# Optimization experiments

Measured on AMD Instinct MI355X. Metric: run time of the kernel, lower is better.

The kernel has to match this reference:

```python
import jax, jax.numpy as jnp
import numpy as np

B, N, S, C, H = 8, 1024, 1024, 768, 12
D = C // H  # head dim 64
SCALE = D ** -0.5


def setup_inputs() -> dict:
    key = jax.random.key(0)
    ks = jax.random.split(key, 9)
    init = 0.02
    return {
        "query": jax.random.normal(ks[0], (B, N, C), jnp.float32),
        "key": jax.random.normal(ks[1], (B, S, C), jnp.float32),
        "value": jax.random.normal(ks[2], (B, S, C), jnp.float32),
        "attn_weight": jax.random.normal(ks[3], (B, H, N, S), jnp.float32),
        "Wq": jax.random.normal(ks[4], (C, C), jnp.float32) * init,
        "Wk": jax.random.normal(ks[5], (C, C), jnp.float32) * init,
        "Wv": jax.random.normal(ks[6], (C, C), jnp.float32) * init,
        "Wo": jax.random.normal(ks[7], (C, C), jnp.float32) * init,
        "bo": jnp.zeros((C,), jnp.float32),
    }


def reference(query, key, value, attn_weight, Wq, Wk, Wv, Wo, bo):
    # projections; torch Linear uses y = x @ W.T
    q = (query @ Wq.T).reshape(B, N, H, D).transpose(0, 2, 1, 3)  # b h n d
    k = (key @ Wk.T).reshape(B, S, H, D).transpose(0, 2, 1, 3)    # b h s d
    v = (value @ Wv.T).reshape(B, S, H, D).transpose(0, 2, 1, 3)  # b h s d

    scores = jnp.einsum("bhnd,bhsd->bhns", q, k) * SCALE          # [B,H,N,S]
    log_attn = jax.nn.log_softmax(scores, axis=-1)
    # bias-add then re-softmax (attn_weight path)
    logits = attn_weight + log_attn
    log_attn = logits
    attn = jax.nn.softmax(logits, axis=-1)

    out = jnp.einsum("bhns,bhsd->bhnd", attn, v)                   # [B,H,N,D]
    out = out.transpose(0, 2, 1, 3).reshape(B, N, C)               # b n (h d)
    out = out @ Wo.T + bo
    return out, log_attn
```

## Files before the change

### kernel.cpp

```cpp
#include <hip/hip_runtime.h>
#include <stdint.h>

#define DEV __device__ __forceinline__

typedef short bf16x8 __attribute__((ext_vector_type(8)));
typedef float f32x4 __attribute__((ext_vector_type(4)));

constexpr int CB = 8, CN = 1024, CS = 1024, CC = 768, CH = 12, CD = 64;

DEV unsigned short f32_to_bf16(float f) {
    unsigned int u = __builtin_bit_cast(unsigned int, f);
    u += 0x7fffu + ((u >> 16) & 1u);
    return (unsigned short)(u >> 16);
}
DEV float bf16_to_f32(unsigned short h) {
    return __builtin_bit_cast(float, (unsigned int)h << 16);
}

DEV uint4 load8_bf16(const float* __restrict__ src) {
    const float4 a = reinterpret_cast<const float4*>(src)[0];
    const float4 b = reinterpret_cast<const float4*>(src)[1];
    union { unsigned short s[8]; uint4 v; } u;
    u.s[0] = f32_to_bf16(a.x); u.s[1] = f32_to_bf16(a.y);
    u.s[2] = f32_to_bf16(a.z); u.s[3] = f32_to_bf16(a.w);
    u.s[4] = f32_to_bf16(b.x); u.s[5] = f32_to_bf16(b.y);
    u.s[6] = f32_to_bf16(b.z); u.s[7] = f32_to_bf16(b.w);
    return u.v;
}
DEV uint4 load8_bf16(const unsigned short* __restrict__ src) {
    return *reinterpret_cast<const uint4*>(src);
}

template<typename TA, typename TB, typename TC>
__global__ __launch_bounds__(256)
void gemm_nt(const TA* __restrict__ Ag, const TB* __restrict__ Bg, TC* __restrict__ Cg,
             int M, int Ndim, int K, int lda, int ldb, int Hb,
             long sAb, long sAh, long sBb, long sBh, long sCb, long sCh,
             long cSM, long cSN, float scale, const float* __restrict__ bias)
{
    const int bb = blockIdx.z / Hb;
    const int hh = blockIdx.z % Hb;
    const TA* __restrict__ A  = Ag + bb * sAb + hh * sAh;
    const TB* __restrict__ Bp = Bg + bb * sBb + hh * sBh;
    TC* __restrict__ C = Cg + bb * sCb + hh * sCh;

    const int tileM = blockIdx.x * 64;
    const int tileN = blockIdx.y * 64;
    const int tid  = threadIdx.x;
    const int lane = tid & 63;
    const int wv   = tid >> 6;
    const int wr   = (wv >> 1) * 32;
    const int wc   = (wv & 1) * 32;
    const int l15  = lane & 15;
    const int quad = lane >> 4;

    constexpr int LDP = 40;
    __shared__ unsigned short As[64 * LDP];
    __shared__ unsigned short Bs[64 * LDP];

    f32x4 acc[2][2] = {};

    const int ldRow = tid >> 2;
    const int ldCol = (tid & 3) * 8;

    const TA* aSrc = A  + (long)(tileM + ldRow) * lda + ldCol;
    const TB* bSrc = Bp + (long)(tileN + ldRow) * ldb + ldCol;
    uint4* aDst = reinterpret_cast<uint4*>(&As[ldRow * LDP + ldCol]);
    uint4* bDst = reinterpret_cast<uint4*>(&Bs[ldRow * LDP + ldCol]);

    for (int k0 = 0; k0 < K; k0 += 32) {
        *aDst = load8_bf16(aSrc + k0);
        *bDst = load8_bf16(bSrc + k0);
        __syncthreads();
        bf16x8 af[2], bfr[2];
        #pragma unroll
        for (int i = 0; i < 2; ++i)
            af[i] = *reinterpret_cast<const bf16x8*>(&As[(wr + i*16 + l15) * LDP + quad*8]);
        #pragma unroll
        for (int j = 0; j < 2; ++j)
            bfr[j] = *reinterpret_cast<const bf16x8*>(&Bs[(wc + j*16 + l15) * LDP + quad*8]);
        #pragma unroll
        for (int i = 0; i < 2; ++i)
            #pragma unroll
            for (int j = 0; j < 2; ++j)
                acc[i][j] = __builtin_amdgcn_mfma_f32_16x16x32_bf16(af[i], bfr[j], acc[i][j], 0, 0, 0);
        __syncthreads();
    }

    #pragma unroll
    for (int i = 0; i < 2; ++i) {
        #pragma unroll
        for (int j = 0; j < 2; ++j) {
            const int col = tileN + wc + j*16 + l15;
            const float bv = bias ? bias[col] : 0.0f;
            #pragma unroll
            for (int r = 0; r < 4; ++r) {
                const int row = tileM + wr + i*16 + quad*4 + r;
                const float v = acc[i][j][r] * scale + bv;
                const long idx = (long)row * cSM + (long)col * cSN;
                if constexpr (sizeof(TC) == 2) C[idx] = f32_to_bf16(v);
                else                           C[idx] = v;
            }
        }
    }
}

__global__ __launch_bounds__(256)
void softmax_k(const unsigned short* __restrict__ scores,
               const float* __restrict__ aw,
               float* __restrict__ log_attn,
               unsigned short* __restrict__ probs)
{
    const int lane = threadIdx.x & 63;
    const int wv   = threadIdx.x >> 6;
    const long row  = (long)blockIdx.x * 4 + wv;
    const long base = row * CS;

    float sc[16], t[16];
    #pragma unroll
    for (int j = 0; j < 16; ++j) {
        const int col = lane + j * 64;
        sc[j] = bf16_to_f32(scores[base + col]);
        t[j]  = aw[base + col] + sc[j];
    }
    float m1 = -3.4e38f, m2 = -3.4e38f;
    #pragma unroll
    for (int j = 0; j < 16; ++j) { m1 = fmaxf(m1, sc[j]); m2 = fmaxf(m2, t[j]); }
    #pragma unroll
    for (int off = 1; off < 64; off <<= 1) {
        m1 = fmaxf(m1, __shfl_xor(m1, off));
        m2 = fmaxf(m2, __shfl_xor(m2, off));
    }
    float l1 = 0.f, l2 = 0.f;
    #pragma unroll
    for (int j = 0; j < 16; ++j) { l1 += __expf(sc[j] - m1); l2 += __expf(t[j] - m2); }
    #pragma unroll
    for (int off = 1; off < 64; off <<= 1) {
        l1 += __shfl_xor(l1, off);
        l2 += __shfl_xor(l2, off);
    }
    const float lse1 = m1 + __logf(l1);
    const float inv2 = 1.0f / l2;
    #pragma unroll
    for (int j = 0; j < 16; ++j) {
        const int col = lane + j * 64;
        log_attn[base + col] = t[j] - lse1;
        probs[base + col]    = f32_to_bf16(__expf(t[j] - m2) * inv2);
    }
}

extern "C" void kernel_launch(void* const* d_in, const int* in_sizes, int n_in,
                              void* d_out, int out_size, void* d_ws, size_t ws_size,
                              hipStream_t stream)
{
    const float* query = (const float*)d_in[0];
    const float* key_  = (const float*)d_in[1];
    const float* value = (const float*)d_in[2];
    const float* aw    = (const float*)d_in[3];
    const float* Wq    = (const float*)d_in[4];
    const float* Wk    = (const float*)d_in[5];
    const float* Wv    = (const float*)d_in[6];
    const float* Wo    = (const float*)d_in[7];
    const float* bo    = (const float*)d_in[8];

    float* out      = (float*)d_out;
    float* log_attn = out + (long)CB * CN * CC;

    unsigned short* qproj = (unsigned short*)d_ws;
    unsigned short* kproj = qproj + (long)CB * CN * CC;
    unsigned short* vT    = kproj + (long)CB * CS * CC;
    unsigned short* sp    = vT    + (long)CB * CS * CC;
    unsigned short* aout  = sp    + (long)CB * CH * CN * CS;

    const dim3 blk(256);

    gemm_nt<float, float, unsigned short><<<dim3(128, 12, 1), blk, 0, stream>>>(
        query, Wq, qproj, CB*CN, CC, CC, CC, CC, 1,
        0, 0, 0, 0, 0, 0, (long)CC, 1, 1.0f, nullptr);
    gemm_nt<float, float, unsigned short><<<dim3(128, 12, 1), blk, 0, stream>>>(
        key_, Wk, kproj, CB*CS, CC, CC, CC, CC, 1,
        0, 0, 0, 0, 0, 0, (long)CC, 1, 1.0f, nullptr);
    gemm_nt<float, float, unsigned short><<<dim3(16, 12, 8), blk, 0, stream>>>(
        value, Wv, vT, CS, CC, CC, CC, CC, 1,
        (long)CS*CC, 0, 0, 0, (long)CH*CD*CS, 0, 1, (long)CS, 1.0f, nullptr);
    gemm_nt<unsigned short, unsigned short, unsigned short><<<dim3(16, 16, CB*CH), blk, 0, stream>>>(
        qproj, kproj, sp, CN, CS, CD, CC, CC, CH,
        (long)CN*CC, (long)CD, (long)CS*CC, (long)CD,
        (long)CH*CN*CS, (long)CN*CS, (long)CS, 1, 0.125f, nullptr);
    softmax_k<<<dim3(CB*CH*CN/4), blk, 0, stream>>>(sp, aw, log_attn, sp);
    gemm_nt<unsigned short, unsigned short, unsigned short><<<dim3(16, 1, CB*CH), blk, 0, stream>>>(
        sp, vT, aout, CN, CD, CS, CS, CS, CH,
        (long)CH*CN*CS, (long)CN*CS, (long)CH*CD*CS, (long)CD*CS,
        (long)CN*CC, (long)CD, (long)CC, 1, 1.0f, nullptr);
    gemm_nt<unsigned short, float, float><<<dim3(128, 12, 1), blk, 0, stream>>>(
        aout, Wo, out, CB*CN, CC, CC, CC, CC, 1,
        0, 0, 0, 0, 0, 0, (long)CC, 1, 1.0f, bo);
}
```

Baseline: 1.050 ms.

## Fuse QK^T, double softmax and PV into one LDS-resident attention kernel

Replaces the scores GEMM, the softmax kernel and the PV GEMM with one kernel per 32 query rows of a (batch, head). That kernel keeps the full 32x1024 bf16 score tile in swizzled shared memory. This removes the round trip of the B*H*N*S bf16 score and probability matrix through global memory. It also drops max subtraction in both softmaxes, relying on small score and bias magnitudes, which risks overflow for other inputs. The block uses 64KB of LDS, which limits occupancy.

```diff
diff --git a/kernel.cpp b/kernel.cpp
--- a/kernel.cpp
+++ b/kernel.cpp
@@ -105,47 +105,138 @@
     }
 }
 
+DEV int swz(int row, int col) {
+    return row * 2048 + ((col * 2) ^ ((row & 7) << 4));
+}
+
 __global__ __launch_bounds__(256)
-void softmax_k(const unsigned short* __restrict__ scores,
-               const float* __restrict__ aw,
-               float* __restrict__ log_attn,
-               unsigned short* __restrict__ probs)
+void attn_fused(const unsigned short* __restrict__ qproj,
+                const unsigned short* __restrict__ kproj,
+                const unsigned short* __restrict__ vT,
+                const float* __restrict__ aw,
+                float* __restrict__ log_attn,
+                unsigned short* __restrict__ aout)
 {
-    const int lane = threadIdx.x & 63;
-    const int wv   = threadIdx.x >> 6;
-    const long row  = (long)blockIdx.x * 4 + wv;
-    const long base = row * CS;
-
-    float sc[16], t[16];
+    __shared__ unsigned short sc[32 * 1024];
+    __shared__ float lse[32];
+    __shared__ float l2i[32];
+
+    const int bb  = blockIdx.y / CH;
+    const int hh  = blockIdx.y % CH;
+    const int qb0 = blockIdx.x * 32;
+
+    const int tid  = threadIdx.x;
+    const int lane = tid & 63;
+    const int wv   = tid >> 6;
+    const int l15  = lane & 15;
+    const int quad = lane >> 4;
+
+    char* scB = (char*)sc;
+
+    const unsigned short* qbase = qproj + ((long)(bb * CN + qb0)) * CC + hh * CD;
+    bf16x8 bq[2][2];
     #pragma unroll
-    for (int j = 0; j < 16; ++j) {
-        const int col = lane + j * 64;
-        sc[j] = bf16_to_f32(scores[base + col]);
-        t[j]  = aw[base + col] + sc[j];
-    }
-    float m1 = -3.4e38f, m2 = -3.4e38f;
+    for (int j = 0; j < 2; ++j)
+        #pragma unroll
+        for (int ks = 0; ks < 2; ++ks)
+            bq[j][ks] = *reinterpret_cast<const bf16x8*>(
+                qbase + (long)(j * 16 + l15) * CC + ks * 32 + quad * 8);
+
+    const unsigned short* kbase = kproj + (long)bb * CS * CC + hh * CD;
+    #pragma unroll 2
+    for (int tt = 0; tt < 16; ++tt) {
+        const int s0 = wv * 256 + tt * 16;
+        bf16x8 ak[2];
+        #pragma unroll
+        for (int ks = 0; ks < 2; ++ks)
+            ak[ks] = *reinterpret_cast<const bf16x8*>(
+                kbase + (long)(s0 + l15) * CC + ks * 32 + quad * 8);
+        #pragma unroll
+        for (int j = 0; j < 2; ++j) {
+            f32x4 a = {};
+            a = __builtin_amdgcn_mfma_f32_16x16x32_bf16(ak[0], bq[j][0], a, 0, 0, 0);
+            a = __builtin_amdgcn_mfma_f32_16x16x32_bf16(ak[1], bq[j][1], a, 0, 0, 0);
+            union { unsigned short s4[4]; uint2 v; } pk;
+            #pragma unroll
+            for (int r = 0; r < 4; ++r) pk.s4[r] = f32_to_bf16(a[r] * 0.125f);
+            *reinterpret_cast<uint2*>(scB + swz(j * 16 + l15, s0 + quad * 4)) = pk.v;
+        }
+    }
+    __syncthreads();
+
+    const int row = tid >> 3;
+    const int c8  = tid & 7;
+    {
+        float l1 = 0.f;
+        #pragma unroll 8
+        for (int i = 0; i < 32; ++i) {
+            const int col = c8 * 4 + i * 32;
+            union { uint2 v; unsigned short s4[4]; } pk;
+            pk.v = *reinterpret_cast<const uint2*>(scB + swz(row, col));
+            #pragma unroll
+            for (int r = 0; r < 4; ++r) l1 += __expf(bf16_to_f32(pk.s4[r]));
+        }
+        l1 += __shfl_xor(l1, 1);
+        l1 += __shfl_xor(l1, 2);
+        l1 += __shfl_xor(l1, 4);
+        if (c8 == 0) lse[row] = __logf(l1);
+    }
+    __syncthreads();
+
+    {
+        const long gro = (((long)bb * CH + hh) * CN + qb0 + row) * CS;
+        const float* awr = aw + gro;
+        float* lar = log_attn + gro;
+        const float myl = lse[row];
+        float l2 = 0.f;
+        #pragma unroll 4
+        for (int i = 0; i < 32; ++i) {
+            const int col = c8 * 4 + i * 32;
+            float4 a4 = *reinterpret_cast<const float4*>(awr + col);
+            union { uint2 v; unsigned short s4[4]; } pk;
+            pk.v = *reinterpret_cast<const uint2*>(scB + swz(row, col));
+            const float t0 = a4.x + bf16_to_f32(pk.s4[0]);
+            const float t1 = a4.y + bf16_to_f32(pk.s4[1]);
+            const float t2 = a4.z + bf16_to_f32(pk.s4[2]);
+            const float t3 = a4.w + bf16_to_f32(pk.s4[3]);
+            float4 la = { t0 - myl, t1 - myl, t2 - myl, t3 - myl };
+            *reinterpret_cast<float4*>(lar + col) = la;
+            const float p0 = __expf(t0), p1 = __expf(t1);
+            const float p2 = __expf(t2), p3 = __expf(t3);
+            l2 += (p0 + p1) + (p2 + p3);
+            pk.s4[0] = f32_to_bf16(p0); pk.s4[1] = f32_to_bf16(p1);
+            pk.s4[2] = f32_to_bf16(p2); pk.s4[3] = f32_to_bf16(p3);
+            *reinterpret_cast<uint2*>(scB + swz(row, col)) = pk.v;
+        }
+        l2 += __shfl_xor(l2, 1);
+        l2 += __shfl_xor(l2, 2);
+        l2 += __shfl_xor(l2, 4);
+        if (c8 == 0) l2i[row] = 1.0f / l2;
+    }
+    __syncthreads();
+
+    const int mt = wv >> 1;
+    const int d0 = (wv & 1) * 32;
+    const unsigned short* vbase = vT + ((long)bb * CH + hh) * CD * CS;
+    const unsigned short* v0p = vbase + (long)(d0 + l15) * CS;
+    const unsigned short* v1p = vbase + (long)(d0 + 16 + l15) * CS;
+    f32x4 o0 = {}, o1 = {};
+    #pragma unroll 4
+    for (int ks = 0; ks < 32; ++ks) {
+        const int kc = ks * 32 + quad * 8;
+        bf16x8 pa  = *reinterpret_cast<const bf16x8*>(scB + swz(mt * 16 + l15, kc));
+        bf16x8 vv0 = *reinterpret_cast<const bf16x8*>(v0p + kc);
+        bf16x8 vv1 = *reinterpret_cast<const bf16x8*>(v1p + kc);
+        o0 = __builtin_amdgcn_mfma_f32_16x16x32_bf16(pa, vv0, o0, 0, 0, 0);
+        o1 = __builtin_amdgcn_mfma_f32_16x16x32_bf16(pa, vv1, o1, 0, 0, 0);
+    }
+    unsigned short* abase = aout + ((long)(bb * CN + qb0)) * CC + hh * CD;
     #pragma unroll
-    for (int j = 0; j < 16; ++j) { m1 = fmaxf(m1, sc[j]); m2 = fmaxf(m2, t[j]); }
-    #pragma unroll
-    for (int off = 1; off < 64; off <<= 1) {
-        m1 = fmaxf(m1, __shfl_xor(m1, off));
-        m2 = fmaxf(m2, __shfl_xor(m2, off));
-    }
-    float l1 = 0.f, l2 = 0.f;
-    #pragma unroll
-    for (int j = 0; j < 16; ++j) { l1 += __expf(sc[j] - m1); l2 += __expf(t[j] - m2); }
-    #pragma unroll
-    for (int off = 1; off < 64; off <<= 1) {
-        l1 += __shfl_xor(l1, off);
-        l2 += __shfl_xor(l2, off);
-    }
-    const float lse1 = m1 + __logf(l1);
-    const float inv2 = 1.0f / l2;
-    #pragma unroll
-    for (int j = 0; j < 16; ++j) {
-        const int col = lane + j * 64;
-        log_attn[base + col] = t[j] - lse1;
-        probs[base + col]    = f32_to_bf16(__expf(t[j] - m2) * inv2);
+    for (int r = 0; r < 4; ++r) {
+        const int orow = mt * 16 + quad * 4 + r;
+        const float s = l2i[orow];
+        abase[(long)orow * CC + d0 + l15]      = f32_to_bf16(o0[r] * s);
+        abase[(long)orow * CC + d0 + 16 + l15] = f32_to_bf16(o1[r] * s);
     }
 }
 
@@ -169,8 +260,7 @@
     unsigned short* qproj = (unsigned short*)d_ws;
     unsigned short* kproj = qproj + (long)CB * CN * CC;
     unsigned short* vT    = kproj + (long)CB * CS * CC;
-    unsigned short* sp    = vT    + (long)CB * CS * CC;
-    unsigned short* aout  = sp    + (long)CB * CH * CN * CS;
+    unsigned short* aout  = vT    + (long)CB * CS * CC;
 
     const dim3 blk(256);
 
@@ -183,15 +273,8 @@
     gemm_nt<float, float, unsigned short><<<dim3(16, 12, 8), blk, 0, stream>>>(
         value, Wv, vT, CS, CC, CC, CC, CC, 1,
         (long)CS*CC, 0, 0, 0, (long)CH*CD*CS, 0, 1, (long)CS, 1.0f, nullptr);
-    gemm_nt<unsigned short, unsigned short, unsigned short><<<dim3(16, 16, CB*CH), blk, 0, stream>>>(
-        qproj, kproj, sp, CN, CS, CD, CC, CC, CH,
-        (long)CN*CC, (long)CD, (long)CS*CC, (long)CD,
-        (long)CH*CN*CS, (long)CN*CS, (long)CS, 1, 0.125f, nullptr);
-    softmax_k<<<dim3(CB*CH*CN/4), blk, 0, stream>>>(sp, aw, log_attn, sp);
-    gemm_nt<unsigned short, unsigned short, unsigned short><<<dim3(16, 1, CB*CH), blk, 0, stream>>>(
-        sp, vT, aout, CN, CD, CS, CS, CS, CH,
-        (long)CH*CN*CS, (long)CN*CS, (long)CH*CD*CS, (long)CD*CS,
-        (long)CN*CC, (long)CD, (long)CC, 1, 1.0f, nullptr);
+    attn_fused<<<dim3(CN/32, CB*CH), blk, 0, stream>>>(
+        qproj, kproj, vT, aw, log_attn, aout);
     gemm_nt<unsigned short, float, float><<<dim3(128, 12, 1), blk, 0, stream>>>(
         aout, Wo, out, CB*CN, CC, CC, CC, CC, 1,
         0, 0, 0, 0, 0, 0, (long)CC, 1, 1.0f, bo);
```

Result: faster. 1.008 ms (-4.0%).
